# Optimization experiments

Measured on AMD Instinct MI355X. Metric: run time of the kernel, lower is better.

Reference implementation:

```python
import jax, jax.numpy as jnp
import numpy as np
from jax import lax

B, T = 64, 2048
RNN_DIM, EMB_DIM, ATT_DIM = 1024, 512, 128
N_FILT, KSIZE = 32, 31
PAD = (KSIZE - 1) // 2


def setup_inputs() -> dict:
    key = jax.random.key(0)
    ks = jax.random.split(key, 9)
    return {
        "query": jax.random.normal(ks[0], (B, RNN_DIM), jnp.float32),
        "processed_memory": jax.random.normal(ks[1], (B, T, ATT_DIM), jnp.float32),
        "attention_weights_cat": jax.random.uniform(ks[2], (B, 2, T), jnp.float32),
        "mask": jax.random.randint(ks[3], (B, T), 0, 2).astype(bool),
        "memory": jax.random.normal(ks[4], (B, T, EMB_DIM), jnp.float32),
        # learned parameters (torch Linear stores weight as [out, in])
        "W_query": jax.random.normal(ks[5], (ATT_DIM, RNN_DIM), jnp.float32) * 0.05,
        "conv_w": jax.random.normal(ks[6], (N_FILT, 2, KSIZE), jnp.float32) * 0.05,
        "W_loc": jax.random.normal(ks[7], (ATT_DIM, N_FILT), jnp.float32) * 0.05,
        "v_w": jax.random.normal(ks[8], (1, ATT_DIM), jnp.float32) * 0.05,
    }


def reference(query, processed_memory, attention_weights_cat, mask, memory,
              W_query, conv_w, W_loc, v_w):
    # processed_query: [B, 1, A]
    processed_query = (query @ W_query.T)[:, None, :]
    # location features: conv over time (2 -> N_FILT channels), same padding
    loc = lax.conv_general_dilated(
        attention_weights_cat, conv_w, window_strides=(1,),
        padding=[(PAD, PAD)], dimension_numbers=("NCH", "OIH", "NCH"))  # [B, F, T]
    processed_loc = jnp.einsum("bft,af->bta", loc, W_loc)  # [B, T, A]
    # additive energies -> [B, T]
    energies = jnp.tanh(processed_loc + processed_memory + processed_query) @ v_w[0]
    energies = jnp.where(mask, -jnp.inf, energies)
    attention_weights = jax.nn.softmax(energies, axis=1)  # [B, T]
    attention_context = jnp.einsum("bt,btd->bd", attention_weights, memory)  # [B, D]
    return attention_context, attention_weights
```

## Files before the change

### kernel.cpp

```cpp
#include <hip/hip_runtime.h>
#include <math.h>

#define B_ 64
#define T_ 2048
#define RNN_DIM 1024
#define EMB_DIM 512
#define ATT_DIM 128
#define N_FILT 32
#define KSIZE 31
#define PAD_ 15
#define TT 64
#define NSLICE 32

__device__ __forceinline__ float fast_tanh(float x) {
    float e = __expf(2.0f * x);
    return 1.0f - 2.0f / (e + 1.0f);
}

__global__ __launch_bounds__(256) void k_pq(const float* __restrict__ query,
                                            const float* __restrict__ Wq,
                                            float* __restrict__ pq) {
    __shared__ float4 q4s[RNN_DIM / 4];
    __shared__ float red[4][64];
    const int b = blockIdx.y;
    const int tid = threadIdx.x;
    q4s[tid] = reinterpret_cast<const float4*>(query + (size_t)b * RNN_DIM)[tid];
    __syncthreads();
    const int al = tid & 63;
    const int rp = tid >> 6;
    const int a  = blockIdx.x * 64 + al;
    const float4* w4 = reinterpret_cast<const float4*>(Wq + (size_t)a * RNN_DIM) + rp * 64;
    float acc = 0.f;
    #pragma unroll 8
    for (int i = 0; i < 64; ++i) {
        float4 w = w4[i];
        float4 q = q4s[rp * 64 + i];
        acc += w.x * q.x + w.y * q.y + w.z * q.z + w.w * q.w;
    }
    red[rp][al] = acc;
    __syncthreads();
    if (tid < 64) {
        float r = red[0][tid] + red[1][tid] + red[2][tid] + red[3][tid];
        pq[b * ATT_DIM + blockIdx.x * 64 + tid] = r;
    }
}

__global__ __launch_bounds__(256) void k_energy(
    const float* __restrict__ att,
    const float* __restrict__ pm,
    const float* __restrict__ cw,
    const float* __restrict__ Wl,
    const float* __restrict__ v,
    const float* __restrict__ pq,
    const int*   __restrict__ mask,
    float* __restrict__ P)
{
    __shared__ float att_s[2][TT + KSIZE - 1];
    __shared__ float loc_s[N_FILT][TT];
    __shared__ float pm_s[TT * (ATT_DIM + 1)];
    __shared__ float ep_s[4][TT];

    const int b   = blockIdx.y;
    const int t0  = blockIdx.x * TT;
    const int tid = threadIdx.x;
    const int lane = tid & 63;
    const int w    = __builtin_amdgcn_readfirstlane(tid >> 6);

    if (tid < 2 * (TT + KSIZE - 1)) {
        int c = tid / (TT + KSIZE - 1);
        int i = tid % (TT + KSIZE - 1);
        int gt = t0 + i - PAD_;
        att_s[c][i] = (gt >= 0 && gt < T_) ? att[(b * 2 + c) * T_ + gt] : 0.f;
    }
    {
        const float4* src4 = reinterpret_cast<const float4*>(
            pm + ((size_t)b * T_ + t0) * ATT_DIM);
        #pragma unroll
        for (int j = 0; j < TT * ATT_DIM / 4 / 256; ++j) {
            int idx = tid + 256 * j;
            int row = idx >> 5;
            int c4  = idx & 31;
            float4 vv = src4[idx];
            float* dst = pm_s + row * (ATT_DIM + 1) + c4 * 4;
            dst[0] = vv.x; dst[1] = vv.y; dst[2] = vv.z; dst[3] = vv.w;
        }
    }
    __syncthreads();

    #pragma unroll
    for (int p = 0; p < 2; ++p) {
        int fb = __builtin_amdgcn_readfirstlane(w * 8 + p * 4);
        float a0 = 0.f, a1 = 0.f, a2 = 0.f, a3 = 0.f;
        #pragma unroll
        for (int c = 0; c < 2; ++c) {
            #pragma unroll
            for (int k = 0; k < KSIZE; ++k) {
                float av = att_s[c][lane + k];
                a0 += av * cw[((fb + 0) * 2 + c) * KSIZE + k];
                a1 += av * cw[((fb + 1) * 2 + c) * KSIZE + k];
                a2 += av * cw[((fb + 2) * 2 + c) * KSIZE + k];
                a3 += av * cw[((fb + 3) * 2 + c) * KSIZE + k];
            }
        }
        loc_s[fb + 0][lane] = a0;
        loc_s[fb + 1][lane] = a1;
        loc_s[fb + 2][lane] = a2;
        loc_s[fb + 3][lane] = a3;
    }
    __syncthreads();

    float lreg[N_FILT];
    #pragma unroll
    for (int f = 0; f < N_FILT; ++f) lreg[f] = loc_s[f][lane];

    const float* pm_row = pm_s + lane * (ATT_DIM + 1);
    const float* pq_row = pq + b * ATT_DIM;
    float eacc = 0.f;
    const int abase = __builtin_amdgcn_readfirstlane(w * 32);
    #pragma unroll 2
    for (int j = 0; j < 32; ++j) {
        int a = abase + j;
        const float* wl_row = Wl + a * N_FILT;
        float pl = 0.f;
        #pragma unroll
        for (int f = 0; f < N_FILT; ++f)
            pl += wl_row[f] * lreg[f];
        float x = pl + pm_row[a] + pq_row[a];
        eacc += fast_tanh(x) * v[a];
    }
    ep_s[w][lane] = eacc;
    __syncthreads();

    if (tid < TT) {
        float e = ep_s[0][tid] + ep_s[1][tid] + ep_s[2][tid] + ep_s[3][tid];
        int t = t0 + tid;
        float p = (mask[b * T_ + t] != 0) ? 0.f : __expf(e);
        P[b * T_ + t] = p;
    }
}

__global__ __launch_bounds__(128) void k_ctx_partial(
    const float* __restrict__ P,
    const float* __restrict__ mem,
    float* __restrict__ part)
{
    const int ts = blockIdx.x, b = blockIdx.y, tid = threadIdx.x;
    const int t0 = ts * (T_ / NSLICE);
    const float4* m4 = reinterpret_cast<const float4*>(mem)
                     + ((size_t)b * T_ + t0) * (EMB_DIM / 4);
    float4 acc = make_float4(0.f, 0.f, 0.f, 0.f);
    #pragma unroll 8
    for (int t = 0; t < T_ / NSLICE; ++t) {
        float wt = P[b * T_ + t0 + t];
        float4 mv = m4[(size_t)t * (EMB_DIM / 4) + tid];
        acc.x += wt * mv.x; acc.y += wt * mv.y;
        acc.z += wt * mv.z; acc.w += wt * mv.w;
    }
    reinterpret_cast<float4*>(part)[((size_t)b * NSLICE + ts) * (EMB_DIM / 4) + tid] = acc;
}

__global__ __launch_bounds__(256) void k_combine(
    const float* __restrict__ part,
    float* __restrict__ W,
    float* __restrict__ ctx)
{
    __shared__ float red[4];
    const int b = blockIdx.x, tid = threadIdx.x;
    float p[T_ / 256];
    float s = 0.f;
    #pragma unroll
    for (int j = 0; j < T_ / 256; ++j) {
        p[j] = W[b * T_ + tid + 256 * j];
        s += p[j];
    }
    #pragma unroll
    for (int off = 32; off >= 1; off >>= 1)
        s += __shfl_xor(s, off, 64);
    if ((tid & 63) == 0) red[tid >> 6] = s;
    __syncthreads();
    const float S = red[0] + red[1] + red[2] + red[3];
    const float inv = 1.0f / S;
    #pragma unroll
    for (int j = 0; j < T_ / 256; ++j)
        W[b * T_ + tid + 256 * j] = p[j] * inv;
    #pragma unroll
    for (int j = 0; j < EMB_DIM / 256; ++j) {
        int d = tid + 256 * j;
        float acc = 0.f;
        #pragma unroll
        for (int ts = 0; ts < NSLICE; ++ts)
            acc += part[((size_t)b * NSLICE + ts) * EMB_DIM + d];
        ctx[b * EMB_DIM + d] = acc * inv;
    }
}

extern "C" void kernel_launch(void* const* d_in, const int* in_sizes, int n_in,
                              void* d_out, int out_size, void* d_ws, size_t ws_size,
                              hipStream_t stream) {
    const float* query = (const float*)d_in[0];
    const float* pm    = (const float*)d_in[1];
    const float* att   = (const float*)d_in[2];
    const int*   mask  = (const int*)d_in[3];
    const float* mem   = (const float*)d_in[4];
    const float* Wq    = (const float*)d_in[5];
    const float* cw    = (const float*)d_in[6];
    const float* Wl    = (const float*)d_in[7];
    const float* vw    = (const float*)d_in[8];

    float* ctx = (float*)d_out;
    float* wts = (float*)d_out + B_ * EMB_DIM;
    float* pq   = (float*)d_ws;
    float* part = pq + B_ * ATT_DIM;

    k_pq         <<<dim3(2, B_),       dim3(256), 0, stream>>>(query, Wq, pq);
    k_energy     <<<dim3(T_/TT, B_),   dim3(256), 0, stream>>>(att, pm, cw, Wl, vw, pq, mask, wts);
    k_ctx_partial<<<dim3(NSLICE, B_),  dim3(128), 0, stream>>>(wts, mem, part);
    k_combine    <<<dim3(B_),          dim3(256), 0, stream>>>(part, wts, ctx);
}
```

Baseline: 455.7 us.

## Fuse context partial accumulation into energy kernel using shared-memory weights

Merges the energy kernel and the context-partial kernel. After computing the unnormalized exp weights for its 64-timestep tile, each block keeps them in shared memory and immediately accumulates weighted memory rows into two partial context vectors. This removes one kernel launch and the global re-read of the weight array. The number of partials per batch doubles, so the combine kernel sums 64 slices instead of 32, and the energy blocks now carry the memory-streaming work, which may lengthen their tail.

```diff
diff --git a/kernel.cpp b/kernel.cpp
--- a/kernel.cpp
+++ b/kernel.cpp
@@ -11,6 +11,7 @@
 #define PAD_ 15
 #define TT 64
 #define NSLICE 32
+#define NPART 64
 
 __device__ __forceinline__ float fast_tanh(float x) {
     float e = __expf(2.0f * x);
@@ -45,7 +46,7 @@
     }
 }
 
-__global__ __launch_bounds__(256) void k_energy(
+__global__ __launch_bounds__(256) void k_fused(
     const float* __restrict__ att,
     const float* __restrict__ pm,
     const float* __restrict__ cw,
@@ -53,15 +54,19 @@
     const float* __restrict__ v,
     const float* __restrict__ pq,
     const int*   __restrict__ mask,
-    float* __restrict__ P)
+    const float* __restrict__ mem,
+    float* __restrict__ P,
+    float* __restrict__ part)
 {
     __shared__ float att_s[2][TT + KSIZE - 1];
     __shared__ float loc_s[N_FILT][TT];
     __shared__ float pm_s[TT * (ATT_DIM + 1)];
     __shared__ float ep_s[4][TT];
+    __shared__ float p_s[TT];
 
     const int b   = blockIdx.y;
-    const int t0  = blockIdx.x * TT;
+    const int ts  = blockIdx.x;
+    const int t0  = ts * TT;
     const int tid = threadIdx.x;
     const int lane = tid & 63;
     const int w    = __builtin_amdgcn_readfirstlane(tid >> 6);
@@ -136,27 +141,24 @@
         int t = t0 + tid;
         float p = (mask[b * T_ + t] != 0) ? 0.f : __expf(e);
         P[b * T_ + t] = p;
-    }
-}
-
-__global__ __launch_bounds__(128) void k_ctx_partial(
-    const float* __restrict__ P,
-    const float* __restrict__ mem,
-    float* __restrict__ part)
-{
-    const int ts = blockIdx.x, b = blockIdx.y, tid = threadIdx.x;
-    const int t0 = ts * (T_ / NSLICE);
+        p_s[tid] = p;
+    }
+    __syncthreads();
+
+    const int g  = tid >> 7;
+    const int d4 = tid & 127;
     const float4* m4 = reinterpret_cast<const float4*>(mem)
-                     + ((size_t)b * T_ + t0) * (EMB_DIM / 4);
+                     + ((size_t)b * T_ + t0 + g * 32) * (EMB_DIM / 4);
     float4 acc = make_float4(0.f, 0.f, 0.f, 0.f);
     #pragma unroll 8
-    for (int t = 0; t < T_ / NSLICE; ++t) {
-        float wt = P[b * T_ + t0 + t];
-        float4 mv = m4[(size_t)t * (EMB_DIM / 4) + tid];
+    for (int i = 0; i < 32; ++i) {
+        float wt = p_s[g * 32 + i];
+        float4 mv = m4[(size_t)i * (EMB_DIM / 4) + d4];
         acc.x += wt * mv.x; acc.y += wt * mv.y;
         acc.z += wt * mv.z; acc.w += wt * mv.w;
     }
-    reinterpret_cast<float4*>(part)[((size_t)b * NSLICE + ts) * (EMB_DIM / 4) + tid] = acc;
+    reinterpret_cast<float4*>(part)[
+        ((size_t)(b * NPART + ts * 2 + g)) * (EMB_DIM / 4) + d4] = acc;
 }
 
 __global__ __launch_bounds__(256) void k_combine(
@@ -188,8 +190,8 @@
         int d = tid + 256 * j;
         float acc = 0.f;
         #pragma unroll
-        for (int ts = 0; ts < NSLICE; ++ts)
-            acc += part[((size_t)b * NSLICE + ts) * EMB_DIM + d];
+        for (int sl = 0; sl < NPART; ++sl)
+            acc += part[((size_t)b * NPART + sl) * EMB_DIM + d];
         ctx[b * EMB_DIM + d] = acc * inv;
     }
 }
@@ -212,8 +214,7 @@
     float* pq   = (float*)d_ws;
     float* part = pq + B_ * ATT_DIM;
 
-    k_pq         <<<dim3(2, B_),       dim3(256), 0, stream>>>(query, Wq, pq);
-    k_energy     <<<dim3(T_/TT, B_),   dim3(256), 0, stream>>>(att, pm, cw, Wl, vw, pq, mask, wts);
-    k_ctx_partial<<<dim3(NSLICE, B_),  dim3(128), 0, stream>>>(wts, mem, part);
-    k_combine    <<<dim3(B_),          dim3(256), 0, stream>>>(part, wts, ctx);
-}
+    k_pq     <<<dim3(2, B_),        dim3(256), 0, stream>>>(query, Wq, pq);
+    k_fused  <<<dim3(NSLICE, B_),   dim3(256), 0, stream>>>(att, pm, cw, Wl, vw, pq, mask, mem, wts, part);
+    k_combine<<<dim3(B_),           dim3(256), 0, stream>>>(part, wts, ctx);
+}
```

New measurement: 456.1 us. No clear change (+0.1%).
